# Kernel optimization log

Measured on AMD Instinct MI355X. Metric: run time of the kernel, lower is better.

Reference implementation:

```python
import jax, jax.numpy as jnp
import numpy as np

D_MODEL = 1024
N_HEADS = 16
HEAD_DIM = D_MODEL // N_HEADS


def setup_inputs() -> dict:
    key = jax.random.key(0)
    k1, k2, k3 = jax.random.split(key, 3)
    x = jax.random.normal(k1, (4, 2048, D_MODEL), dtype=jnp.float32)
    # per-head qkv Linear (bias=False): torch weight [3*head_dim, d_model];
    # store transposed and stacked over heads: [H, d_model, 3*head_dim]
    w_qkv = jax.random.normal(k2, (N_HEADS, D_MODEL, 3 * HEAD_DIM), dtype=jnp.float32) * (1.0 / np.sqrt(D_MODEL))
    # output Linear (bias=False), stored transposed: [d_model, d_model]
    w_out = jax.random.normal(k3, (D_MODEL, D_MODEL), dtype=jnp.float32) * (1.0 / np.sqrt(D_MODEL))
    return {"x": x, "w_qkv": w_qkv, "w_out": w_out}


def reference(x, w_qkv, w_out):
    hd = HEAD_DIM
    # all heads' qkv in one contraction: [B, H, S, 3*hd]
    qkv = jnp.einsum("bsd,hde->bhse", x, w_qkv)
    q, k, v = qkv[..., :hd], qkv[..., hd:2 * hd], qkv[..., 2 * hd:]
    scale = 1.0 / hd  # NOTE: original scales by 1/dk, not 1/sqrt(dk)
    scores = jnp.einsum("bhqe,bhke->bhqk", q, k) * scale
    attn = jax.nn.softmax(scores, axis=-1)
    z = jnp.einsum("bhqk,bhke->bhqe", attn, v)  # [B, H, S, hd]
    # concat heads along feature dim (head order = list order)
    b, h, s, _ = z.shape
    z = jnp.transpose(z, (0, 2, 1, 3)).reshape(b, s, h * hd)
    return z @ w_out
```

## Files before the change

kernel.cpp:

```cpp
#include <hip/hip_runtime.h>
#include <hip/hip_bf16.h>

typedef unsigned short u16;
typedef __attribute__((ext_vector_type(4))) float f32x4;
typedef __attribute__((ext_vector_type(16))) float f32x16;
typedef __attribute__((ext_vector_type(8))) short s16x8;
typedef __attribute__((ext_vector_type(4))) unsigned short u16x4;

static __device__ __forceinline__ u16 f32_to_bf16(float f) {
    union { float f; unsigned u; } v; v.f = f;
    unsigned r = v.u + 0x7FFF + ((v.u >> 16) & 1);
    return (u16)(r >> 16);
}

static __device__ __forceinline__ unsigned cvt_pk_bf16(float lo, float hi) {
    unsigned r;
    asm("v_cvt_pk_bf16_f32 %0, %1, %2" : "=v"(r) : "v"(lo), "v"(hi));
    return r;
}

static __device__ __forceinline__ void pswap2(unsigned &a, unsigned &b) {
#if defined(__has_builtin) && __has_builtin(__builtin_amdgcn_permlane32_swap)
    auto r = __builtin_amdgcn_permlane32_swap(a, b, false, false);
    a = r[0]; b = r[1];
#else
    asm volatile("v_permlane32_swap_b32 %0, %1" : "+v"(a), "+v"(b));
#endif
}

static __device__ __forceinline__ float xhalf_sum(float x) {
    unsigned a = __float_as_uint(x), b = a;
    pswap2(a, b);
    return __uint_as_float(a) + __uint_as_float(b);
}

static __device__ __forceinline__ float fexp2(float x) {
#if defined(__has_builtin) && __has_builtin(__builtin_amdgcn_exp2f)
    return __builtin_amdgcn_exp2f(x);
#else
    return exp2f(x);
#endif
}

#define GLOAD_LDS16(gptr, lptr) \
    __builtin_amdgcn_global_load_lds((const __attribute__((address_space(1))) void*)(gptr), \
                                     (__attribute__((address_space(3))) void*)(lptr), 16, 0, 0)

__global__ void cvt_all(const float* __restrict__ x, u16* __restrict__ xb,
                        const float* __restrict__ wq, u16* __restrict__ wqT,
                        const float* __restrict__ wo, u16* __restrict__ woT) {
    __shared__ float tile[32][33];
    const int bid = blockIdx.x;
    if (bid < 8192) {
        int i = (bid * 256 + threadIdx.x) * 4;
        f32x4 v = *(const f32x4*)(x + i);
        u16x4 o;
        o.x = f32_to_bf16(v.x); o.y = f32_to_bf16(v.y);
        o.z = f32_to_bf16(v.z); o.w = f32_to_bf16(v.w);
        *(u16x4*)(xb + i) = o;
    } else if (bid < 8192 + 3072) {
        const int b = bid - 8192;
        const int kb = b & 31, eb = (b >> 5) % 6, h = b / 192;
        const int xl = threadIdx.x & 31, y = threadIdx.x >> 5;
#pragma unroll
        for (int j = 0; j < 4; ++j) {
            int kl = y + j * 8;
            tile[kl][xl] = wq[((size_t)(h * 1024 + kb * 32 + kl)) * 192 + eb * 32 + xl];
        }
        __syncthreads();
#pragma unroll
        for (int j = 0; j < 4; ++j) {
            int el = y + j * 8;
            wqT[((size_t)(h * 192 + eb * 32 + el)) * 1024 + kb * 32 + xl] = f32_to_bf16(tile[xl][el]);
        }
    } else {
        const int b = bid - 8192 - 3072;
        const int kb = b & 31, nb = b >> 5;
        const int xl = threadIdx.x & 31, y = threadIdx.x >> 5;
#pragma unroll
        for (int j = 0; j < 4; ++j) {
            int kl = y + j * 8;
            tile[kl][xl] = wo[((size_t)(kb * 32 + kl)) * 1024 + nb * 32 + xl];
        }
        __syncthreads();
#pragma unroll
        for (int j = 0; j < 4; ++j) {
            int nl = y + j * 8;
            woT[((size_t)(nb * 32 + nl)) * 1024 + kb * 32 + xl] = f32_to_bf16(tile[xl][nl]);
        }
    }
}


#define SWZ4(r) (((r) & 3) ^ (((r) >> 2) & 3))

template <int EPI>
__global__ __launch_bounds__(256, 3)
void gemm_bt(const u16* __restrict__ A, const u16* __restrict__ B,
             float* __restrict__ Cf, u16* __restrict__ Qb, u16* __restrict__ Kb,
             u16* __restrict__ Vt, int M, int N, int K) {
    __shared__ __align__(16) u16 lA[3 * 128 * 32];
    __shared__ __align__(16) u16 lB[3 * 128 * 32];

    const int t = threadIdx.x;
    const int lane = t & 63;
    const int wave = t >> 6;
    const int wr = wave >> 1, wc = wave & 1;
    const int l15 = lane & 15, g = lane >> 4;

    const int nwg = gridDim.x;
    const int cpx = nwg >> 3;
    const int orig = blockIdx.x;
    const int logical = (orig & 7) * cpx + (orig >> 3);

    const int nbx = N >> 7;
    const int bx = logical % nbx, by = logical / nbx;
    const int bm = by << 7, bn = bx << 7;

    f32x4 acc[4][4] = {};

    const int sr0 = t >> 2;
    const int ss  = t & 3;

    const u16* Abase = A + (size_t)bm * K;
    const u16* Bbase = B + (size_t)bn * K;

    int aoff[4], boff[4];
#pragma unroll
    for (int i = 0; i < 4; ++i) {
        int ra = wr * 64 + i * 16 + l15;
        aoff[i] = (ra * 4 + (g ^ SWZ4(ra))) * 8;
        int rb = wc * 64 + i * 16 + l15;
        boff[i] = (rb * 4 + (g ^ SWZ4(rb))) * 8;
    }

#define GSTAGE(bb, kt) do { \
    _Pragma("unroll") \
    for (int c = 0; c < 2; ++c) { \
        int r = sr0 + 64 * c; \
        int cl = ss ^ SWZ4(r); \
        GLOAD_LDS16(Abase + (size_t)r * K + (kt) + cl * 8, &lA[(bb) + (r * 4 + ss) * 8]); \
        GLOAD_LDS16(Bbase + (size_t)r * K + (kt) + cl * 8, &lB[(bb) + (r * 4 + ss) * 8]); \
    } } while (0)

#define GEMM_STEP(B0, B2, KT, DO_STAGE, DO_SYNC, WAIT4)                        \
  {                                                                            \
    if (DO_STAGE) GSTAGE((B2) * 4096, (KT));                                   \
    s16x8 a0 = *(const s16x8*)&lA[(B0) * 4096 + aoff[0]];                      \
    s16x8 a1 = *(const s16x8*)&lA[(B0) * 4096 + aoff[1]];                      \
    s16x8 a2 = *(const s16x8*)&lA[(B0) * 4096 + aoff[2]];                      \
    s16x8 a3 = *(const s16x8*)&lA[(B0) * 4096 + aoff[3]];                      \
    s16x8 b0 = *(const s16x8*)&lB[(B0) * 4096 + boff[0]];                      \
    s16x8 b1 = *(const s16x8*)&lB[(B0) * 4096 + boff[1]];                      \
    s16x8 b2 = *(const s16x8*)&lB[(B0) * 4096 + boff[2]];                      \
    s16x8 b3 = *(const s16x8*)&lB[(B0) * 4096 + boff[3]];                      \
    acc[0][0] = __builtin_amdgcn_mfma_f32_16x16x32_bf16(b0, a0, acc[0][0], 0, 0, 0); \
    acc[0][1] = __builtin_amdgcn_mfma_f32_16x16x32_bf16(b1, a0, acc[0][1], 0, 0, 0); \
    acc[0][2] = __builtin_amdgcn_mfma_f32_16x16x32_bf16(b2, a0, acc[0][2], 0, 0, 0); \
    acc[0][3] = __builtin_amdgcn_mfma_f32_16x16x32_bf16(b3, a0, acc[0][3], 0, 0, 0); \
    acc[1][0] = __builtin_amdgcn_mfma_f32_16x16x32_bf16(b0, a1, acc[1][0], 0, 0, 0); \
    acc[1][1] = __builtin_amdgcn_mfma_f32_16x16x32_bf16(b1, a1, acc[1][1], 0, 0, 0); \
    acc[1][2] = __builtin_amdgcn_mfma_f32_16x16x32_bf16(b2, a1, acc[1][2], 0, 0, 0); \
    acc[1][3] = __builtin_amdgcn_mfma_f32_16x16x32_bf16(b3, a1, acc[1][3], 0, 0, 0); \
    acc[2][0] = __builtin_amdgcn_mfma_f32_16x16x32_bf16(b0, a2, acc[2][0], 0, 0, 0); \
    acc[2][1] = __builtin_amdgcn_mfma_f32_16x16x32_bf16(b1, a2, acc[2][1], 0, 0, 0); \
    acc[2][2] = __builtin_amdgcn_mfma_f32_16x16x32_bf16(b2, a2, acc[2][2], 0, 0, 0); \
    acc[2][3] = __builtin_amdgcn_mfma_f32_16x16x32_bf16(b3, a2, acc[2][3], 0, 0, 0); \
    acc[3][0] = __builtin_amdgcn_mfma_f32_16x16x32_bf16(b0, a3, acc[3][0], 0, 0, 0); \
    acc[3][1] = __builtin_amdgcn_mfma_f32_16x16x32_bf16(b1, a3, acc[3][1], 0, 0, 0); \
    acc[3][2] = __builtin_amdgcn_mfma_f32_16x16x32_bf16(b2, a3, acc[3][2], 0, 0, 0); \
    acc[3][3] = __builtin_amdgcn_mfma_f32_16x16x32_bf16(b3, a3, acc[3][3], 0, 0, 0); \
    if (DO_SYNC) {                                                             \
      if (WAIT4) { asm volatile("s_waitcnt vmcnt(4)" ::: "memory"); }          \
      else       { asm volatile("s_waitcnt vmcnt(0)" ::: "memory"); }          \
      __builtin_amdgcn_s_barrier();                                            \
      __builtin_amdgcn_sched_barrier(0);                                       \
    }                                                                          \
  }

    GSTAGE(0, 0);
    GSTAGE(4096, 32);
    asm volatile("s_waitcnt vmcnt(4)" ::: "memory");
    __builtin_amdgcn_s_barrier();
    __builtin_amdgcn_sched_barrier(0);

#pragma unroll 1
    for (int tt = 0; tt < 30; tt += 3) {
        GEMM_STEP(0, 2, (tt + 2) << 5, true, true, true);
        GEMM_STEP(1, 0, (tt + 3) << 5, true, true, true);
        GEMM_STEP(2, 1, (tt + 4) << 5, true, true, true);
    }
    GEMM_STEP(0, 0, 0, false, true, false);
    GEMM_STEP(1, 0, 0, false, false, false);
#undef GEMM_STEP
#undef GSTAGE

    if constexpr (EPI == 0) {
#pragma unroll
        for (int i = 0; i < 4; ++i) {
            int m = bm + wr * 64 + i * 16 + l15;
#pragma unroll
            for (int j = 0; j < 4; ++j) {
                int n0 = bn + wc * 64 + j * 16 + g * 4;
                *(f32x4*)&Cf[(size_t)m * N + n0] = acc[i][j];
            }
        }
    } else {
        const float qscale = 0.022542110013890054f;
#pragma unroll
        for (int j = 0; j < 4; ++j) {
            int n0 = bn + wc * 64 + j * 16 + g * 4;
            int h = n0 / 192;
            int e0 = n0 - h * 192;
#pragma unroll
            for (int i = 0; i < 4; ++i) {
                int m = bm + wr * 64 + i * 16 + l15;
                int bb = m >> 11, s = m & 2047;
                int bh = bb * 16 + h;
                if (e0 < 64) {
                    u16x4 q;
#pragma unroll
                    for (int r = 0; r < 4; ++r) q[r] = f32_to_bf16(acc[i][j][r] * qscale);
                    *(u16x4*)&Qb[((size_t)bh * 2048 + s) * 64 + e0] = q;
                } else if (e0 < 128) {
                    u16x4 kk;
#pragma unroll
                    for (int r = 0; r < 4; ++r) kk[r] = f32_to_bf16(acc[i][j][r]);
                    *(u16x4*)&Kb[((size_t)bh * 2048 + s) * 64 + (e0 - 64)] = kk;
                } else {
#pragma unroll
                    for (int r = 0; r < 4; ++r)
                        Vt[((size_t)bh * 64 + (e0 - 128 + r)) * 2048 + s] = f32_to_bf16(acc[i][j][r]);
                }
            }
        }
    }
}


static __device__ __forceinline__ void soft_pack32(f32x16& p0, float& l,
                                                   s16x8& pv0, s16x8& pv1) {
    float rs0 = 0.f, rs1 = 0.f, rs2 = 0.f, rs3 = 0.f;
#pragma unroll
    for (int r = 0; r < 16; r += 4) {
        p0[r]     = fexp2(p0[r]);     rs0 += p0[r];
        p0[r + 1] = fexp2(p0[r + 1]); rs1 += p0[r + 1];
        p0[r + 2] = fexp2(p0[r + 2]); rs2 += p0[r + 2];
        p0[r + 3] = fexp2(p0[r + 3]); rs3 += p0[r + 3];
    }
    l += xhalf_sum((rs0 + rs1) + (rs2 + rs3));

    unsigned c0 = cvt_pk_bf16(p0[0],  p0[1]);
    unsigned c1 = cvt_pk_bf16(p0[2],  p0[3]);
    unsigned c2 = cvt_pk_bf16(p0[4],  p0[5]);
    unsigned c3 = cvt_pk_bf16(p0[6],  p0[7]);
    unsigned c4 = cvt_pk_bf16(p0[8],  p0[9]);
    unsigned c5 = cvt_pk_bf16(p0[10], p0[11]);
    unsigned c6 = cvt_pk_bf16(p0[12], p0[13]);
    unsigned c7 = cvt_pk_bf16(p0[14], p0[15]);
    pswap2(c0, c2); pswap2(c1, c3);
    pswap2(c4, c6); pswap2(c5, c7);
    union { unsigned u[8]; s16x8 v[2]; } pa;
    pa.u[0] = c0; pa.u[1] = c1; pa.u[2] = c2; pa.u[3] = c3;
    pa.u[4] = c4; pa.u[5] = c5; pa.u[6] = c6; pa.u[7] = c7;
    pv0 = pa.v[0]; pv1 = pa.v[1];
}

__global__ __launch_bounds__(256, 4)
void attn32(const u16* __restrict__ Qb, const u16* __restrict__ Kb,
            const u16* __restrict__ Vt, u16* __restrict__ Zb) {
    __shared__ __align__(16) u16 lK[3 * 2048];
    __shared__ __align__(16) u16 lV[3 * 2048];
    __shared__ float lds_l[4][32];

    const int t = threadIdx.x;
    const int lane = t & 63;
    const int w = t >> 6;
    const int l31 = lane & 31, hi = lane >> 5;
    const int r7 = l31 & 7;

    const int orig = blockIdx.x;
    const int logical = (orig & 7) * 128 + (orig >> 3);
    const int bh = logical >> 4;
    const int qt = logical & 15;
    const int q0 = qt * 128 + w * 32;

    const u16* Kbh = Kb + (size_t)bh * 2048 * 64;
    const u16* Vbh = Vt + (size_t)bh * 64 * 2048;

    const u16* Qp = Qb + ((size_t)bh * 2048 + q0 + l31) * 64 + hi * 8;
    const s16x8 qf0 = *(const s16x8*)(Qp);
    const s16x8 qf1 = *(const s16x8*)(Qp + 16);
    const s16x8 qf2 = *(const s16x8*)(Qp + 32);
    const s16x8 qf3 = *(const s16x8*)(Qp + 48);

    const int ka0 = l31 * 64 + (((0 + hi) ^ r7) << 3);
    const int ka1 = l31 * 64 + (((2 + hi) ^ r7) << 3);
    const int ka2 = l31 * 64 + (((4 + hi) ^ r7) << 3);
    const int ka3 = l31 * 64 + (((6 + hi) ^ r7) << 3);
    const int s3  = (l31 >> 1) & 3;
    const int va0 = l31 * 32 + (((0 + hi) ^ s3) << 3);
    const int va1 = l31 * 32 + (((2 + hi) ^ s3) << 3);

    f32x16 o0 = {}, o1 = {};
    float l = 0.f;

#define STAGE(bb, kvn) do { \
    int kr_ = w * 8 + (lane >> 3); \
    GLOAD_LDS16(Kbh + (size_t)((kvn) + kr_) * 64 + (((lane & 7) ^ (lane >> 3)) * 8), \
                &lK[(bb) + w * 512 + lane * 8]); \
    int vr_ = w * 16 + (lane >> 2); \
    GLOAD_LDS16(Vbh + (size_t)vr_ * 2048 + (kvn) + (((lane & 3) ^ ((lane >> 3) & 3)) * 8), \
                &lV[(bb) + w * 512 + lane * 8]); \
    } while (0)

#define ATTN_STEP(B0, B2, KVN, DO_STAGE, DO_SYNC, WAIT2)                             \
  {                                                                                  \
    if (DO_STAGE) STAGE((B2) * 2048, (KVN));                                         \
    f32x16 p0 = {};                                                                  \
    __builtin_amdgcn_s_setprio(1);                                                   \
    {                                                                                \
      s16x8 kf;                                                                      \
      kf = *(const s16x8*)&lK[(B0) * 2048 + ka0];                                    \
      p0 = __builtin_amdgcn_mfma_f32_32x32x16_bf16(kf, qf0, p0, 0, 0, 0);            \
      kf = *(const s16x8*)&lK[(B0) * 2048 + ka1];                                    \
      p0 = __builtin_amdgcn_mfma_f32_32x32x16_bf16(kf, qf1, p0, 0, 0, 0);            \
      kf = *(const s16x8*)&lK[(B0) * 2048 + ka2];                                    \
      p0 = __builtin_amdgcn_mfma_f32_32x32x16_bf16(kf, qf2, p0, 0, 0, 0);            \
      kf = *(const s16x8*)&lK[(B0) * 2048 + ka3];                                    \
      p0 = __builtin_amdgcn_mfma_f32_32x32x16_bf16(kf, qf3, p0, 0, 0, 0);            \
    }                                                                                \
    __builtin_amdgcn_s_setprio(0);                                                   \
    s16x8 pv0, pv1;                                                                  \
    soft_pack32(p0, l, pv0, pv1);                                                    \
    __builtin_amdgcn_s_setprio(1);                                                   \
    {                                                                                \
      s16x8 vf;                                                                      \
      vf = *(const s16x8*)&lV[(B0) * 2048 + va0];                                    \
      o0 = __builtin_amdgcn_mfma_f32_32x32x16_bf16(pv0, vf, o0, 0, 0, 0);            \
      vf = *(const s16x8*)&lV[(B0) * 2048 + va0 + 1024];                             \
      o1 = __builtin_amdgcn_mfma_f32_32x32x16_bf16(pv0, vf, o1, 0, 0, 0);            \
      vf = *(const s16x8*)&lV[(B0) * 2048 + va1];                                    \
      o0 = __builtin_amdgcn_mfma_f32_32x32x16_bf16(pv1, vf, o0, 0, 0, 0);            \
      vf = *(const s16x8*)&lV[(B0) * 2048 + va1 + 1024];                             \
      o1 = __builtin_amdgcn_mfma_f32_32x32x16_bf16(pv1, vf, o1, 0, 0, 0);            \
    }                                                                                \
    __builtin_amdgcn_s_setprio(0);                                                   \
    if (DO_SYNC) {                                                                   \
      if (WAIT2) { asm volatile("s_waitcnt vmcnt(2)" ::: "memory"); }                \
      else       { asm volatile("s_waitcnt vmcnt(0)" ::: "memory"); }                \
      __builtin_amdgcn_s_barrier();                                                  \
      __builtin_amdgcn_sched_barrier(0);                                             \
    }                                                                                \
  }

    STAGE(0, 0);
    STAGE(2048, 32);
    asm volatile("s_waitcnt vmcnt(2)" ::: "memory");
    __builtin_amdgcn_s_barrier();
    __builtin_amdgcn_sched_barrier(0);

#pragma unroll 1
    for (int tt = 0; tt < 60; tt += 3) {
        ATTN_STEP(0, 2, (tt + 2) << 5, true, true, true);
        ATTN_STEP(1, 0, (tt + 3) << 5, true, true, true);
        ATTN_STEP(2, 1, (tt + 4) << 5, true, true, true);
    }
    ATTN_STEP(0, 2, 62 << 5, true, true, true);
    ATTN_STEP(1, 0, 63 << 5, true, true, true);
    ATTN_STEP(2, 0, 0, false, true, false);
    ATTN_STEP(0, 0, 0, false, false, false);
#undef ATTN_STEP
#undef STAGE

    if (lane < 32) lds_l[w][l31] = l;
    __syncthreads();

    const int b = bh >> 4, h = bh & 15;
#pragma unroll
    for (int r = 0; r < 16; ++r) {
        int qrow = (r & 3) + 8 * (r >> 2) + 4 * hi;
        float inv = 1.0f / lds_l[w][qrow];
        size_t rowbase = ((size_t)(b * 2048 + q0 + qrow)) * 1024 + h * 64 + l31;
        Zb[rowbase]      = f32_to_bf16(o0[r] * inv);
        Zb[rowbase + 32] = f32_to_bf16(o1[r] * inv);
    }
}


extern "C" void kernel_launch(void* const* d_in, const int* in_sizes, int n_in,
                              void* d_out, int out_size, void* d_ws, size_t ws_size,
                              hipStream_t stream) {
    const float* x     = (const float*)d_in[0];
    const float* w_qkv = (const float*)d_in[1];
    const float* w_out = (const float*)d_in[2];
    float* out = (float*)d_out;

    char* ws = (char*)d_ws;
    u16* xb  = (u16*)ws; ws += (size_t)8192 * 1024 * 2;
    u16* wqT = (u16*)ws; ws += (size_t)3072 * 1024 * 2;
    u16* woT = (u16*)ws; ws += (size_t)1024 * 1024 * 2;
    u16* Qb  = (u16*)ws; ws += (size_t)64 * 2048 * 64 * 2;
    u16* Kb  = (u16*)ws; ws += (size_t)64 * 2048 * 64 * 2;
    u16* Vt  = (u16*)ws; ws += (size_t)64 * 2048 * 64 * 2;
    u16* Zb  = (u16*)ws; ws += (size_t)8192 * 1024 * 2;

    cvt_all<<<dim3(8192 + 3072 + 1024), dim3(256), 0, stream>>>(x, xb, w_qkv, wqT, w_out, woT);

    gemm_bt<1><<<dim3(64 * 24), dim3(256), 0, stream>>>(xb, wqT, nullptr, Qb, Kb, Vt,
                                                        8192, 3072, 1024);
    attn32<<<dim3(1024), dim3(256), 0, stream>>>(Qb, Kb, Vt, Zb);
    gemm_bt<0><<<dim3(64 * 8), dim3(256), 0, stream>>>(Zb, woT, out, nullptr, nullptr, nullptr,
                                                       8192, 1024, 1024);
}
```

Before: 193.0 us.

## Split attention KV range across two wave groups with LDS reduction

The attention kernel now launches 512 threads per block: two groups of four waves each process half of the KV sequence (split-K) for the same 128 queries, then combine partial outputs and row sums through shared memory before normalizing. The KV pipeline is changed from triple buffering to double buffering, with staging issued after the barrier. The aim is more waves in flight and shorter serial loops per wave to hide latency. The cost is an extra LDS reduction step and a full vmcnt(0) wait every step, and the double buffer may expose more load latency. Softmax has no max subtraction, so a simple sum of the partials stays correct.

```diff
diff --git a/kernel.cpp b/kernel.cpp
--- a/kernel.cpp
+++ b/kernel.cpp
@@ -266,16 +266,20 @@
     pv0 = pa.v[0]; pv1 = pa.v[1];
 }
 
-__global__ __launch_bounds__(256, 4)
+__global__ __launch_bounds__(512, 8)
 void attn32(const u16* __restrict__ Qb, const u16* __restrict__ Kb,
             const u16* __restrict__ Vt, u16* __restrict__ Zb) {
-    __shared__ __align__(16) u16 lK[3 * 2048];
-    __shared__ __align__(16) u16 lV[3 * 2048];
-    __shared__ float lds_l[4][32];
+    __shared__ __align__(16) unsigned char smem[32768];
+    __shared__ float lds_l[8][32];
+
+    u16* lK = (u16*)smem;
+    u16* lV = (u16*)(smem + 16384);
+    float* scr = (float*)smem;
 
     const int t = threadIdx.x;
     const int lane = t & 63;
     const int w = t >> 6;
+    const int qg = w & 3, kh = w >> 2;
     const int l31 = lane & 31, hi = lane >> 5;
     const int r7 = l31 & 7;
 
@@ -283,10 +287,13 @@
     const int logical = (orig & 7) * 128 + (orig >> 3);
     const int bh = logical >> 4;
     const int qt = logical & 15;
-    const int q0 = qt * 128 + w * 32;
-
-    const u16* Kbh = Kb + (size_t)bh * 2048 * 64;
-    const u16* Vbh = Vt + (size_t)bh * 64 * 2048;
+    const int q0 = qt * 128 + qg * 32;
+
+    const u16* Kbh = Kb + ((size_t)bh * 2048 + kh * 1024) * 64;
+    const u16* Vbh = Vt + (size_t)bh * 64 * 2048 + kh * 1024;
+
+    u16* lKw = lK + kh * 4096;
+    u16* lVw = lV + kh * 4096;
 
     const u16* Qp = Qb + ((size_t)bh * 2048 + q0 + l31) * 64 + hi * 8;
     const s16x8 qf0 = *(const s16x8*)(Qp);
@@ -305,29 +312,28 @@
     f32x16 o0 = {}, o1 = {};
     float l = 0.f;
 
-#define STAGE(bb, kvn) do { \
-    int kr_ = w * 8 + (lane >> 3); \
-    GLOAD_LDS16(Kbh + (size_t)((kvn) + kr_) * 64 + (((lane & 7) ^ (lane >> 3)) * 8), \
-                &lK[(bb) + w * 512 + lane * 8]); \
-    int vr_ = w * 16 + (lane >> 2); \
-    GLOAD_LDS16(Vbh + (size_t)vr_ * 2048 + (kvn) + (((lane & 3) ^ ((lane >> 3) & 3)) * 8), \
-                &lV[(bb) + w * 512 + lane * 8]); \
-    } while (0)
-
-#define ATTN_STEP(B0, B2, KVN, DO_STAGE, DO_SYNC, WAIT2)                             \
+#define STAGE(bufe, tile) do { \
+    int gr = (qg << 3) + (lane >> 3); \
+    GLOAD_LDS16(Kbh + (size_t)(((tile) << 5) + gr) * 64 + (((lane & 7) ^ (lane >> 3)) << 3), \
+                lKw + (bufe) * 2048 + (qg << 9) + lane * 8); \
+    int vr = (qg << 4) + (lane >> 2); \
+    GLOAD_LDS16(Vbh + (size_t)vr * 2048 + ((tile) << 5) + (((lane & 3) ^ ((lane >> 3) & 3)) << 3), \
+                lVw + (bufe) * 2048 + (qg << 9) + lane * 8); \
+} while (0)
+
+#define ATTN_STEP(B, T2, DO_STAGE, DO_SYNC)                                          \
   {                                                                                  \
-    if (DO_STAGE) STAGE((B2) * 2048, (KVN));                                         \
     f32x16 p0 = {};                                                                  \
     __builtin_amdgcn_s_setprio(1);                                                   \
     {                                                                                \
       s16x8 kf;                                                                      \
-      kf = *(const s16x8*)&lK[(B0) * 2048 + ka0];                                    \
+      kf = *(const s16x8*)&lKw[(B) * 2048 + ka0];                                    \
       p0 = __builtin_amdgcn_mfma_f32_32x32x16_bf16(kf, qf0, p0, 0, 0, 0);            \
-      kf = *(const s16x8*)&lK[(B0) * 2048 + ka1];                                    \
+      kf = *(const s16x8*)&lKw[(B) * 2048 + ka1];                                    \
       p0 = __builtin_amdgcn_mfma_f32_32x32x16_bf16(kf, qf1, p0, 0, 0, 0);            \
-      kf = *(const s16x8*)&lK[(B0) * 2048 + ka2];                                    \
+      kf = *(const s16x8*)&lKw[(B) * 2048 + ka2];                                    \
       p0 = __builtin_amdgcn_mfma_f32_32x32x16_bf16(kf, qf2, p0, 0, 0, 0);            \
-      kf = *(const s16x8*)&lK[(B0) * 2048 + ka3];                                    \
+      kf = *(const s16x8*)&lKw[(B) * 2048 + ka3];                                    \
       p0 = __builtin_amdgcn_mfma_f32_32x32x16_bf16(kf, qf3, p0, 0, 0, 0);            \
     }                                                                                \
     __builtin_amdgcn_s_setprio(0);                                                   \
@@ -336,54 +342,69 @@
     __builtin_amdgcn_s_setprio(1);                                                   \
     {                                                                                \
       s16x8 vf;                                                                      \
-      vf = *(const s16x8*)&lV[(B0) * 2048 + va0];                                    \
+      vf = *(const s16x8*)&lVw[(B) * 2048 + va0];                                    \
       o0 = __builtin_amdgcn_mfma_f32_32x32x16_bf16(pv0, vf, o0, 0, 0, 0);            \
-      vf = *(const s16x8*)&lV[(B0) * 2048 + va0 + 1024];                             \
+      vf = *(const s16x8*)&lVw[(B) * 2048 + va0 + 1024];                             \
       o1 = __builtin_amdgcn_mfma_f32_32x32x16_bf16(pv0, vf, o1, 0, 0, 0);            \
-      vf = *(const s16x8*)&lV[(B0) * 2048 + va1];                                    \
+      vf = *(const s16x8*)&lVw[(B) * 2048 + va1];                                    \
       o0 = __builtin_amdgcn_mfma_f32_32x32x16_bf16(pv1, vf, o0, 0, 0, 0);            \
-      vf = *(const s16x8*)&lV[(B0) * 2048 + va1 + 1024];                             \
+      vf = *(const s16x8*)&lVw[(B) * 2048 + va1 + 1024];                             \
       o1 = __builtin_amdgcn_mfma_f32_32x32x16_bf16(pv1, vf, o1, 0, 0, 0);            \
     }                                                                                \
     __builtin_amdgcn_s_setprio(0);                                                   \
     if (DO_SYNC) {                                                                   \
-      if (WAIT2) { asm volatile("s_waitcnt vmcnt(2)" ::: "memory"); }                \
-      else       { asm volatile("s_waitcnt vmcnt(0)" ::: "memory"); }                \
+      asm volatile("s_waitcnt vmcnt(0)" ::: "memory");                               \
       __builtin_amdgcn_s_barrier();                                                  \
       __builtin_amdgcn_sched_barrier(0);                                             \
     }                                                                                \
+    if (DO_STAGE) STAGE(B, T2);                                                      \
   }
 
     STAGE(0, 0);
-    STAGE(2048, 32);
+    STAGE(1, 1);
     asm volatile("s_waitcnt vmcnt(2)" ::: "memory");
     __builtin_amdgcn_s_barrier();
     __builtin_amdgcn_sched_barrier(0);
 
 #pragma unroll 1
-    for (int tt = 0; tt < 60; tt += 3) {
-        ATTN_STEP(0, 2, (tt + 2) << 5, true, true, true);
-        ATTN_STEP(1, 0, (tt + 3) << 5, true, true, true);
-        ATTN_STEP(2, 1, (tt + 4) << 5, true, true, true);
-    }
-    ATTN_STEP(0, 2, 62 << 5, true, true, true);
-    ATTN_STEP(1, 0, 63 << 5, true, true, true);
-    ATTN_STEP(2, 0, 0, false, true, false);
-    ATTN_STEP(0, 0, 0, false, false, false);
+    for (int tt = 0; tt < 30; tt += 2) {
+        ATTN_STEP(0, tt + 2, true, true);
+        ATTN_STEP(1, tt + 3, true, true);
+    }
+    ATTN_STEP(0, 0, false, true);
+    ATTN_STEP(1, 0, false, false);
 #undef ATTN_STEP
 #undef STAGE
 
     if (lane < 32) lds_l[w][l31] = l;
     __syncthreads();
 
-    const int b = bh >> 4, h = bh & 15;
-#pragma unroll
-    for (int r = 0; r < 16; ++r) {
-        int qrow = (r & 3) + 8 * (r >> 2) + 4 * hi;
-        float inv = 1.0f / lds_l[w][qrow];
-        size_t rowbase = ((size_t)(b * 2048 + q0 + qrow)) * 1024 + h * 64 + l31;
-        Zb[rowbase]      = f32_to_bf16(o0[r] * inv);
-        Zb[rowbase + 32] = f32_to_bf16(o1[r] * inv);
+    if (w >= 4) {
+        float* sp = scr + (qg * 32) * 64 + lane;
+#pragma unroll
+        for (int r = 0; r < 16; ++r) {
+            sp[r * 64]        = o0[r];
+            sp[(16 + r) * 64] = o1[r];
+        }
+    }
+    __syncthreads();
+
+    if (w < 4) {
+        const float* sp = scr + (qg * 32) * 64 + lane;
+#pragma unroll
+        for (int r = 0; r < 16; ++r) {
+            o0[r] += sp[r * 64];
+            o1[r] += sp[(16 + r) * 64];
+        }
+        const int b = bh >> 4, h = bh & 15;
+#pragma unroll
+        for (int r = 0; r < 16; ++r) {
+            int qrow = (r & 3) + 8 * (r >> 2) + 4 * hi;
+            float inv = 1.0f / (lds_l[w][qrow] + lds_l[w + 4][qrow]);
+            size_t rowbase = ((size_t)(b * 2048 + q0 + qrow)) * 1024 + h * 64 + l31;
+            Zb[rowbase]      = f32_to_bf16(o0[r] * inv);
+            Zb[rowbase + 32] = f32_to_bf16(o1[r] * inv);
+        }
     }
 }
 
@@ -409,7 +430,7 @@
 
     gemm_bt<1><<<dim3(64 * 24), dim3(256), 0, stream>>>(xb, wqT, nullptr, Qb, Kb, Vt,
                                                         8192, 3072, 1024);
-    attn32<<<dim3(1024), dim3(256), 0, stream>>>(Qb, Kb, Vt, Zb);
+    attn32<<<dim3(1024), dim3(512), 0, stream>>>(Qb, Kb, Vt, Zb);
     gemm_bt<0><<<dim3(64 * 8), dim3(256), 0, stream>>>(Zb, woT, out, nullptr, nullptr, nullptr,
                                                        8192, 1024, 1024);
 }
```

Result: slower. 367.8 us (+90.6%).
